# Kernel tuning notes

Measured on AMD Instinct MI355X. Metric: run time of the kernel, lower is better.

Reference implementation:

```python
import jax, jax.numpy as jnp
import numpy as np

N = 100000      # nodes
E = 1600000     # edges (before self loops)
F_IN = 128
HID = 128
C = 32
L = 3


def setup_inputs() -> dict:
    key = jax.random.key(0)
    k = jax.random.split(key, 7)
    x = jax.random.normal(k[0], (N, F_IN), dtype=jnp.float32)
    edge_index = jax.random.randint(k[1], (2, E), 0, N)
    norm = jax.random.uniform(k[2], (E + N,), dtype=jnp.float32)  # per-edge Jaccard norm incl. self loops
    # layer weights stored as [in, out] (equivalent to nn.Linear weight transposed)
    Ws = jax.random.normal(k[3], (L, HID, HID), dtype=jnp.float32) * (1.0 / np.sqrt(HID))
    bs = jnp.zeros((L, HID), dtype=jnp.float32)
    Wc = jax.random.normal(k[4], (HID, C), dtype=jnp.float32) * (1.0 / np.sqrt(HID))
    bc = jnp.zeros((C,), dtype=jnp.float32)
    return {"x": x, "edge_index": edge_index, "norm": norm,
            "Ws": Ws, "bs": bs, "Wc": Wc, "bc": bc}


def reference(x, edge_index, norm, Ws, bs, Wc, bc):
    n = x.shape[0]
    loops = jnp.arange(n, dtype=edge_index.dtype)
    src = jnp.concatenate([edge_index[0], loops])  # [E+N]
    dst = jnp.concatenate([edge_index[1], loops])  # [E+N]
    for i in range(L):
        h = x @ Ws[i]                               # [N, HID] linear (no bias)
        msg = norm[:, None] * h[src]                # edge-wise gather + scale
        agg = jax.ops.segment_max(msg, dst, num_segments=n)  # scatter-max
        agg = jnp.where(jnp.isneginf(agg), 0.0, agg)          # empty segments -> 0
        x = jax.nn.relu(agg + bs[i])
    logits = x @ Wc + bc
    return jax.nn.log_softmax(logits, axis=-1)
```

## Files before the change

kernel.cpp:

```cpp
#include <hip/hip_runtime.h>
#include <hip/hip_fp16.h>
#include <math.h>

#define HID 128
#define NCLS 32
#define BCAP 12288
#define SCAP 9728
#define SLCSH 14

typedef _Float16 half8 __attribute__((ext_vector_type(8)));
typedef _Float16 h2 __attribute__((ext_vector_type(2)));
typedef float f32x4 __attribute__((ext_vector_type(4)));

union hbits_u { unsigned short u; _Float16 f; };

__device__ __forceinline__ void gload_lds16(const void* g, void* l) {
  __builtin_amdgcn_global_load_lds(
      (const __attribute__((address_space(1))) void*)g,
      (__attribute__((address_space(3))) void*)l, 16, 0, 0);
}

__device__ __forceinline__ h2 pk_max(h2 a, h2 b) {
  return __builtin_elementwise_max(a, b);
}

__device__ __forceinline__ _Float16 dec_w(unsigned e) {
  hbits_u u; u.u = (unsigned short)((e >> 16) & 0xFFFEu);
  return u.f;
}

__global__ void k_prep_w(const float* __restrict__ Ws, __half* __restrict__ Wt,
                         int total) {
  int i = blockIdx.x * blockDim.x + threadIdx.x;
  if (i >= total) return;
  int l = i >> 14, r = i & 16383;
  int nn = r >> 7, k = r & 127;
  Wt[i] = __float2half_rn(Ws[(l << 14) + k * HID + nn]);
}

__global__ __launch_bounds__(1024) void k_bin(const int* __restrict__ ei,
                                              const float* __restrict__ norm,
                                              int* __restrict__ bucket_cur,
                                              int2* __restrict__ bins,
                                              int E, int T) {
  __shared__ int bcnt[256];
  __shared__ int bbase[256];
  int tid = threadIdx.x;
  if (tid < 256) bcnt[tid] = 0;
  __syncthreads();
  int base = blockIdx.x * 8192;
  int2 ent[8];
  int bk[8];
  #pragma unroll
  for (int i = 0; i < 8; ++i) {
    int e = base + (i << 10) + tid;
    bk[i] = -1;
    if (e < T) {
      int src, dst;
      if (e < E) { src = ei[e]; dst = ei[E + e]; } else { src = dst = e - E; }
      bk[i] = dst >> 9;
      ent[i] = make_int2(src | ((dst & 511) << 17), __float_as_int(norm[e]));
      atomicAdd(&bcnt[bk[i]], 1);
    }
  }
  __syncthreads();
  if (tid < 256) {
    int c = bcnt[tid];
    bbase[tid] = c ? atomicAdd(&bucket_cur[tid], c) : 0;
    bcnt[tid] = 0;
  }
  __syncthreads();
  #pragma unroll
  for (int i = 0; i < 8; ++i) {
    if (bk[i] >= 0) {
      int pos = bbase[bk[i]] + atomicAdd(&bcnt[bk[i]], 1);
      bins[(size_t)bk[i] * BCAP + pos] = ent[i];
    }
  }
}

__global__ __launch_bounds__(256) void k_bscan(const int* __restrict__ bucket_cur,
                                               int* __restrict__ bucket_off, int nb) {
  __shared__ int a[256];
  int tid = threadIdx.x;
  int orig = (tid < nb) ? bucket_cur[tid] : 0;
  a[tid] = orig;
  __syncthreads();
  for (int d = 1; d < 256; d <<= 1) {
    int t = (tid >= d) ? a[tid - d] : 0;
    __syncthreads();
    a[tid] += t;
    __syncthreads();
  }
  if (tid < nb) bucket_off[tid] = a[tid] - orig;
  if (tid == nb - 1) bucket_off[nb] = a[tid];
}

__global__ __launch_bounds__(1024) void k_sortbucket(
    const int2* __restrict__ bins, const int* __restrict__ bucket_off,
    unsigned* __restrict__ csr4, int* __restrict__ row_off, int n, int nb) {
  __shared__ unsigned sorted[SCAP];
  __shared__ int cnt_[4096];
  __shared__ int wsum[16];
  int b = blockIdx.x, tid = threadIdx.x;
  int goff = bucket_off[b];
  int cnt = bucket_off[b + 1] - goff;
  if (cnt > SCAP) cnt = SCAP;
  const int2* src = bins + (size_t)b * BCAP;
  int2 myent[10];
  int mykey[10];
  #pragma unroll
  for (int i = 0; i < 10; ++i) {
    int j = tid + (i << 10);
    if (j < cnt) {
      myent[i] = src[j];
      int s = myent[i].x & 0x1FFFF;
      int dl = ((unsigned)myent[i].x) >> 17;
      mykey[i] = (dl << 3) | (s >> SLCSH);
    }
  }
  #pragma unroll
  for (int i = 0; i < 4; ++i) cnt_[tid + (i << 10)] = 0;
  __syncthreads();
  #pragma unroll
  for (int i = 0; i < 10; ++i) {
    int j = tid + (i << 10);
    if (j < cnt) atomicAdd(&cnt_[mykey[i]], 1);
  }
  __syncthreads();
  int base = tid << 2;
  int l0 = cnt_[base], l1 = cnt_[base + 1], l2 = cnt_[base + 2], l3 = cnt_[base + 3];
  int s0 = l0 + l1 + l2 + l3;
  int lane = tid & 63, wid = tid >> 6;
  int incl = s0;
  #pragma unroll
  for (int d = 1; d < 64; d <<= 1) {
    int t = __shfl_up(incl, d, 64);
    if (lane >= d) incl += t;
  }
  if (lane == 63) wsum[wid] = incl;
  __syncthreads();
  if (wid == 0 && lane < 16) {
    int wv = wsum[lane];
    int winc = wv;
    #pragma unroll
    for (int d = 1; d < 16; d <<= 1) {
      int t = __shfl_up(winc, d, 16);
      if (lane >= d) winc += t;
    }
    wsum[lane] = winc - wv;
  }
  __syncthreads();
  int excl = incl - s0 + wsum[wid];
  cnt_[base]     = excl;
  cnt_[base + 1] = excl + l0;
  cnt_[base + 2] = excl + l0 + l1;
  cnt_[base + 3] = excl + l0 + l1 + l2;
  __syncthreads();
  int node = (b << 9) + tid;
  if (tid < 512 && node < n) row_off[node] = goff + cnt_[tid << 3];
  if (b == nb - 1 && tid == 0) row_off[n] = bucket_off[nb];
  __syncthreads();
  #pragma unroll
  for (int i = 0; i < 10; ++i) {
    int j = tid + (i << 10);
    if (j < cnt) {
      int pos = atomicAdd(&cnt_[mykey[i]], 1);
      if (pos < SCAP) {
        __half h = __float2half_rn(__int_as_float(myent[i].y));
        unsigned short hb = *(unsigned short*)&h;
        sorted[pos] = (unsigned)(myent[i].x & 0x1FFFF) | ((unsigned)(hb >> 1) << 17);
      }
    }
  }
  __syncthreads();
  for (int j = tid; j < cnt; j += 1024) csr4[goff + j] = sorted[j];
}

__global__ __launch_bounds__(256) void k_gemm_mfma(const __half* __restrict__ X,
                                                   const __half* __restrict__ Wl,
                                                   __half* __restrict__ H, int n) {
  __shared__ char lds[49152];
  char* ldsW = lds;
  char* ldsX = lds + 32768;
  int tid = threadIdx.x, lane = tid & 63, w = tid >> 6;
  int row0 = blockIdx.x * 64;
  int rows = n - row0; if (rows > 64) rows = 64;
  int vbytes = rows << 8;

  #pragma unroll
  for (int it = 0; it < 8; ++it) {
    int d = (w << 13) + (it << 10) + (lane << 4);
    int src = d ^ (((d >> 8) & 7) << 4);
    gload_lds16((const char*)Wl + src, ldsW + (w << 13) + (it << 10));
  }
  #pragma unroll
  for (int it = 0; it < 4; ++it) {
    int d = (w << 12) + (it << 10) + (lane << 4);
    if (d < vbytes) {
      int src = d ^ (((d >> 8) & 7) << 4);
      gload_lds16((const char*)X + ((size_t)row0 << 8) + src,
                  ldsX + (w << 12) + (it << 10));
    }
  }
  __syncthreads();

  int l15 = lane & 15, lhi = lane >> 4;
  half8 a[4];
  #pragma unroll
  for (int s = 0; s < 4; ++s) {
    int m = (w << 4) + l15;
    int d = (m << 8) + (s << 6) + (lhi << 4);
    a[s] = *(const half8*)(ldsX + (d ^ ((m & 7) << 4)));
  }
  __syncthreads();
  f32x4 acc[8] = {};
  #pragma unroll
  for (int s = 0; s < 4; ++s) {
    #pragma unroll
    for (int t = 0; t < 8; ++t) {
      int nn = (t << 4) + l15;
      int d = (nn << 8) + (s << 6) + (lhi << 4);
      half8 b = *(const half8*)(ldsW + (d ^ ((nn & 7) << 4)));
      acc[t] = __builtin_amdgcn_mfma_f32_16x16x32_f16(a[s], b, acc[t], 0, 0, 0);
    }
  }
  #pragma unroll
  for (int t = 0; t < 8; ++t) {
    #pragma unroll
    for (int r = 0; r < 4; ++r) {
      int row = (w << 4) + (lhi << 2) + r;
      int byt = (row << 8) + (t << 5) + (l15 << 1);
      *(__half*)(ldsX + (byt ^ ((row & 7) << 4))) = __float2half_rn(acc[t][r]);
    }
  }
  __syncthreads();
  #pragma unroll
  for (int it = 0; it < 4; ++it) {
    int g = ((it << 8) + tid) << 4;
    if (g < vbytes) {
      uint4 v = *(const uint4*)(ldsX + (g ^ (((g >> 8) & 7) << 4)));
      *(uint4*)((char*)H + ((size_t)row0 << 8) + g) = v;
    }
  }
}

__global__ __launch_bounds__(256) void k_gemm_mfma_f32(const float* __restrict__ X,
                                                       const __half* __restrict__ Wl,
                                                       __half* __restrict__ H, int n) {
  __shared__ char lds[65536];
  char* ldsW = lds;
  char* ldsX = lds + 32768;
  int tid = threadIdx.x, lane = tid & 63, w = tid >> 6;
  int row0 = blockIdx.x * 64;
  int rows = n - row0; if (rows > 64) rows = 64;
  int vbytes32 = rows << 9;
  int vbytes = rows << 8;

  #pragma unroll
  for (int it = 0; it < 8; ++it) {
    int d = (w << 13) + (it << 10) + (lane << 4);
    int src = d ^ (((d >> 8) & 7) << 4);
    gload_lds16((const char*)Wl + src, ldsW + (w << 13) + (it << 10));
  }
  #pragma unroll
  for (int it = 0; it < 8; ++it) {
    int d = (w << 13) + (it << 10) + (lane << 4);
    if (d < vbytes32) {
      int src = d ^ (((d >> 9) & 7) << 4);
      gload_lds16((const char*)X + ((size_t)row0 << 9) + src,
                  ldsX + (w << 13) + (it << 10));
    }
  }
  __syncthreads();

  int l15 = lane & 15, lhi = lane >> 4;
  half8 a[4];
  #pragma unroll
  for (int s = 0; s < 4; ++s) {
    int m = (w << 4) + l15;
    int d0 = (m << 9) + (s << 7) + (lhi << 5);
    int x0 = d0 ^ (((d0 >> 9) & 7) << 4);
    int d1 = d0 + 16;
    int x1 = d1 ^ (((d1 >> 9) & 7) << 4);
    float4 lo = *(const float4*)(ldsX + x0);
    float4 hi = *(const float4*)(ldsX + x1);
    half8 af;
    af[0] = (_Float16)lo.x; af[1] = (_Float16)lo.y;
    af[2] = (_Float16)lo.z; af[3] = (_Float16)lo.w;
    af[4] = (_Float16)hi.x; af[5] = (_Float16)hi.y;
    af[6] = (_Float16)hi.z; af[7] = (_Float16)hi.w;
    a[s] = af;
  }
  __syncthreads();
  f32x4 acc[8] = {};
  #pragma unroll
  for (int s = 0; s < 4; ++s) {
    #pragma unroll
    for (int t = 0; t < 8; ++t) {
      int nn = (t << 4) + l15;
      int d = (nn << 8) + (s << 6) + (lhi << 4);
      half8 b = *(const half8*)(ldsW + (d ^ ((nn & 7) << 4)));
      acc[t] = __builtin_amdgcn_mfma_f32_16x16x32_f16(a[s], b, acc[t], 0, 0, 0);
    }
  }
  #pragma unroll
  for (int t = 0; t < 8; ++t) {
    #pragma unroll
    for (int r = 0; r < 4; ++r) {
      int row = (w << 4) + (lhi << 2) + r;
      int byt = (row << 8) + (t << 5) + (l15 << 1);
      *(__half*)(ldsX + (byt ^ ((row & 7) << 4))) = __float2half_rn(acc[t][r]);
    }
  }
  __syncthreads();
  #pragma unroll
  for (int it = 0; it < 4; ++it) {
    int g = ((it << 8) + tid) << 4;
    if (g < vbytes) {
      uint4 v = *(const uint4*)(ldsX + (g ^ (((g >> 8) & 7) << 4)));
      *(uint4*)((char*)H + ((size_t)row0 << 8) + g) = v;
    }
  }
}

__global__ __launch_bounds__(256) void k_aggregate(
    const __half* __restrict__ H, const int* __restrict__ row_off,
    const unsigned* __restrict__ csr4, const float* __restrict__ bias,
    __half* __restrict__ Xout, int n) {
  int node = (int)((blockIdx.x * blockDim.x + threadIdx.x) >> 6);
  if (node >= n) return;
  int lane = threadIdx.x & 63;
  int q = lane >> 4, l4 = lane & 15;
  int beg = row_off[node], end = row_off[node + 1];
  const char* Hb = (const char*)H + (l4 << 4);
  const unsigned NEG = 0xFC00FC00u;
  h2 m0 = *(const h2*)&NEG, m1 = m0, m2 = m0, m3 = m0;
  int j = beg + q;
  for (; j + 12 < end; j += 16) {
    unsigned e0 = csr4[j], e1 = csr4[j + 4], e2 = csr4[j + 8], e3 = csr4[j + 12];
    _Float16 w0 = dec_w(e0), w1 = dec_w(e1), w2 = dec_w(e2), w3 = dec_w(e3);
    uint4 r0 = *(const uint4*)(Hb + ((size_t)(e0 & 0x1FFFF) << 8));
    uint4 r1 = *(const uint4*)(Hb + ((size_t)(e1 & 0x1FFFF) << 8));
    uint4 r2 = *(const uint4*)(Hb + ((size_t)(e2 & 0x1FFFF) << 8));
    uint4 r3 = *(const uint4*)(Hb + ((size_t)(e3 & 0x1FFFF) << 8));
    m0 = pk_max(m0, *(h2*)&r0.x * w0);
    m1 = pk_max(m1, *(h2*)&r0.y * w0);
    m2 = pk_max(m2, *(h2*)&r0.z * w0);
    m3 = pk_max(m3, *(h2*)&r0.w * w0);
    m0 = pk_max(m0, *(h2*)&r1.x * w1);
    m1 = pk_max(m1, *(h2*)&r1.y * w1);
    m2 = pk_max(m2, *(h2*)&r1.z * w1);
    m3 = pk_max(m3, *(h2*)&r1.w * w1);
    m0 = pk_max(m0, *(h2*)&r2.x * w2);
    m1 = pk_max(m1, *(h2*)&r2.y * w2);
    m2 = pk_max(m2, *(h2*)&r2.z * w2);
    m3 = pk_max(m3, *(h2*)&r2.w * w2);
    m0 = pk_max(m0, *(h2*)&r3.x * w3);
    m1 = pk_max(m1, *(h2*)&r3.y * w3);
    m2 = pk_max(m2, *(h2*)&r3.z * w3);
    m3 = pk_max(m3, *(h2*)&r3.w * w3);
  }
  for (; j < end; j += 4) {
    unsigned e0 = csr4[j];
    _Float16 w0 = dec_w(e0);
    uint4 r0 = *(const uint4*)(Hb + ((size_t)(e0 & 0x1FFFF) << 8));
    m0 = pk_max(m0, *(h2*)&r0.x * w0);
    m1 = pk_max(m1, *(h2*)&r0.y * w0);
    m2 = pk_max(m2, *(h2*)&r0.z * w0);
    m3 = pk_max(m3, *(h2*)&r0.w * w0);
  }
  #pragma unroll
  for (int d = 16; d <= 32; d <<= 1) {
    unsigned u0 = __shfl_xor(*(unsigned*)&m0, d, 64);
    unsigned u1 = __shfl_xor(*(unsigned*)&m1, d, 64);
    unsigned u2 = __shfl_xor(*(unsigned*)&m2, d, 64);
    unsigned u3 = __shfl_xor(*(unsigned*)&m3, d, 64);
    m0 = pk_max(m0, *(h2*)&u0);
    m1 = pk_max(m1, *(h2*)&u1);
    m2 = pk_max(m2, *(h2*)&u2);
    m3 = pk_max(m3, *(h2*)&u3);
  }
  if (q == 0) {
    float f0x = (float)m0.x, f0y = (float)m0.y;
    float f1x = (float)m1.x, f1y = (float)m1.y;
    float f2x = (float)m2.x, f2y = (float)m2.y;
    float f3x = (float)m3.x, f3y = (float)m3.y;
    if (end == beg) {
      f0x=f0y=f1x=f1y=f2x=f2y=f3x=f3y = 0.f;
    }
    float4 b0 = ((const float4*)bias)[l4 << 1];
    float4 b1 = ((const float4*)bias)[(l4 << 1) + 1];
    __half2 o0 = __floats2half2_rn(fmaxf(f0x + b0.x, 0.f), fmaxf(f0y + b0.y, 0.f));
    __half2 o1 = __floats2half2_rn(fmaxf(f1x + b0.z, 0.f), fmaxf(f1y + b0.w, 0.f));
    __half2 o2 = __floats2half2_rn(fmaxf(f2x + b1.x, 0.f), fmaxf(f2y + b1.y, 0.f));
    __half2 o3 = __floats2half2_rn(fmaxf(f3x + b1.z, 0.f), fmaxf(f3y + b1.w, 0.f));
    uint4 ov = make_uint4(*(unsigned*)&o0, *(unsigned*)&o1,
                          *(unsigned*)&o2, *(unsigned*)&o3);
    *(uint4*)((char*)Xout + ((size_t)node << 8) + (l4 << 4)) = ov;
  }
}

__global__ __launch_bounds__(256) void k_classifier(
    const __half* __restrict__ X, const float* __restrict__ Wc,
    const float* __restrict__ bc, float* __restrict__ out, int n) {
  __shared__ float sW[HID * NCLS];
  __shared__ float sx[8][HID];
  int tid = threadIdx.x;
  #pragma unroll
  for (int i = 0; i < 4; ++i)
    ((float4*)sW)[tid + 256 * i] = ((const float4*)Wc)[tid + 256 * i];
  int node0 = blockIdx.x * 8;
  {
    int r = tid >> 5, c = (tid & 31) << 2;
    if (node0 + r < n) {
      __half2 p0 = *(const __half2*)&X[(size_t)(node0 + r) * HID + c];
      __half2 p1 = *(const __half2*)&X[(size_t)(node0 + r) * HID + c + 2];
      float2 f0 = __half22float2(p0), f1 = __half22float2(p1);
      sx[r][c] = f0.x; sx[r][c + 1] = f0.y; sx[r][c + 2] = f1.x; sx[r][c + 3] = f1.y;
    }
  }
  __syncthreads();
  int g = tid >> 5, c = tid & 31;
  int node = node0 + g;
  if (node >= n) return;
  float acc = bc[c];
  #pragma unroll 8
  for (int k = 0; k < HID; ++k)
    acc = fmaf(sx[g][k], sW[k * NCLS + c], acc);
  float m = acc;
  #pragma unroll
  for (int off = 16; off; off >>= 1) m = fmaxf(m, __shfl_xor(m, off, 32));
  float e = expf(acc - m);
  float s = e;
  #pragma unroll
  for (int off = 16; off; off >>= 1) s += __shfl_xor(s, off, 32);
  out[(size_t)node * NCLS + c] = acc - m - logf(s);
}

extern "C" void kernel_launch(void* const* d_in, const int* in_sizes, int n_in,
                              void* d_out, int out_size, void* d_ws, size_t ws_size,
                              hipStream_t stream) {
  const float* x    = (const float*)d_in[0];
  const int*   ei   = (const int*)d_in[1];
  const float* norm = (const float*)d_in[2];
  const float* Ws   = (const float*)d_in[3];
  const float* bs   = (const float*)d_in[4];
  const float* Wc   = (const float*)d_in[5];
  const float* bc   = (const float*)d_in[6];
  float* out = (float*)d_out;

  const int N = in_sizes[0] / HID;
  const int E = in_sizes[1] / 2;
  const int L = in_sizes[3] / (HID * HID);
  const int T = E + N;
  const int NB = (N + 511) >> 9;

  char* p = (char*)d_ws;
  auto alloc = [&](size_t bytes) {
    char* r = p; p += (bytes + 255) & ~(size_t)255; return r;
  };
  __half*   xb0        = (__half*)alloc((size_t)N * HID * 2);
  __half*   xb1        = (__half*)alloc((size_t)N * HID * 2);
  __half*   hbuf       = (__half*)alloc((size_t)N * HID * 2);
  __half*   Wt         = (__half*)alloc((size_t)L * HID * HID * 2);
  int*      row_off    = (int*)alloc(((size_t)N + 1) * 4);
  int*      bucket_cur = (int*)alloc(256 * 4);
  int*      bucket_off = (int*)alloc(257 * 4);
  int2*     bins       = (int2*)alloc((size_t)NB * BCAP * 8);
  unsigned* csr4       = (unsigned*)alloc((size_t)T * 4);
  (void)ws_size; (void)n_in; (void)out_size;

  hipMemsetAsync(bucket_cur, 0, 256 * 4, stream);
  k_prep_w<<<(L * HID * HID + 255) / 256, 256, 0, stream>>>(Ws, Wt, L * HID * HID);
  k_bin<<<(T + 8191) / 8192, 1024, 0, stream>>>(ei, norm, bucket_cur, bins, E, T);
  k_bscan<<<1, 256, 0, stream>>>(bucket_cur, bucket_off, NB);
  k_sortbucket<<<NB, 1024, 0, stream>>>(bins, bucket_off, csr4, row_off, N, NB);

  const int GB = (N + 63) / 64;
  k_gemm_mfma_f32<<<GB, 256, 0, stream>>>(x, Wt, hbuf, N);
  k_aggregate<<<(N + 3) / 4, 256, 0, stream>>>(
      hbuf, row_off, csr4, bs, xb0, N);
  k_gemm_mfma<<<GB, 256, 0, stream>>>(xb0, Wt + (size_t)HID * HID, hbuf, N);
  k_aggregate<<<(N + 3) / 4, 256, 0, stream>>>(
      hbuf, row_off, csr4, bs + HID, xb1, N);
  k_gemm_mfma<<<GB, 256, 0, stream>>>(xb1, Wt + (size_t)2 * HID * HID, hbuf, N);
  k_aggregate<<<(N + 3) / 4, 256, 0, stream>>>(
      hbuf, row_off, csr4, bs + 2 * HID, xb0, N);
  k_classifier<<<(N + 7) / 8, 256, 0, stream>>>(xb0, Wc, bc, out, N);
}
```

Measured before the change: 313.6 us.

## Fuse classifier into last aggregation, fold bucket scan into sort, drop source sub-sort

Merges the final aggregation with the classifier and log-softmax, so each node's 128-wide feature stays in registers and the last hidden activation buffer is never written or re-read. The separate single-block bucket scan kernel is removed: every sort block now computes the prefix over the bucket counts itself. The within-bucket sort key no longer sub-sorts each destination's edges by source slice, which makes sorting cheaper but may reduce gather locality in the aggregation. The classifier weights are pre-transposed in the weight-prep kernel so the fused kernel can do the projection with per-lane partial dot products and cross-lane shuffle reductions.

```diff
diff --git a/kernel.cpp b/kernel.cpp
--- a/kernel.cpp
+++ b/kernel.cpp
@@ -6,7 +6,6 @@
 #define NCLS 32
 #define BCAP 12288
 #define SCAP 9728
-#define SLCSH 14
 
 typedef _Float16 half8 __attribute__((ext_vector_type(8)));
 typedef _Float16 h2 __attribute__((ext_vector_type(2)));
@@ -29,13 +28,19 @@
   return u.f;
 }
 
-__global__ void k_prep_w(const float* __restrict__ Ws, __half* __restrict__ Wt,
-                         int total) {
+__global__ void k_prep_w(const float* __restrict__ Ws, const float* __restrict__ Wc,
+                         __half* __restrict__ Wt, float* __restrict__ Wct,
+                         int totalW, int totalC) {
   int i = blockIdx.x * blockDim.x + threadIdx.x;
-  if (i >= total) return;
-  int l = i >> 14, r = i & 16383;
-  int nn = r >> 7, k = r & 127;
-  Wt[i] = __float2half_rn(Ws[(l << 14) + k * HID + nn]);
+  if (i < totalW) {
+    int l = i >> 14, r = i & 16383;
+    int nn = r >> 7, k = r & 127;
+    Wt[i] = __float2half_rn(Ws[(l << 14) + k * HID + nn]);
+  } else if (i < totalW + totalC) {
+    int j = i - totalW;
+    int c = j >> 7, ch = j & 127;
+    Wct[j] = Wc[ch * NCLS + c];
+  }
 }
 
 __global__ __launch_bounds__(1024) void k_bin(const int* __restrict__ ei,
@@ -79,97 +84,74 @@
   }
 }
 
-__global__ __launch_bounds__(256) void k_bscan(const int* __restrict__ bucket_cur,
-                                               int* __restrict__ bucket_off, int nb) {
-  __shared__ int a[256];
-  int tid = threadIdx.x;
-  int orig = (tid < nb) ? bucket_cur[tid] : 0;
-  a[tid] = orig;
+__global__ __launch_bounds__(1024) void k_sortbucket(
+    const int2* __restrict__ bins, const int* __restrict__ bucket_cur,
+    unsigned* __restrict__ csr4, int* __restrict__ row_off,
+    int n, int nb, int T) {
+  __shared__ unsigned sorted[SCAP];
+  __shared__ int scnt[512];
+  __shared__ int wsum[8];
+  __shared__ int bscan[256];
+  int b = blockIdx.x, tid = threadIdx.x;
+  if (tid < 256) bscan[tid] = (tid < nb) ? bucket_cur[tid] : 0;
   __syncthreads();
   for (int d = 1; d < 256; d <<= 1) {
-    int t = (tid >= d) ? a[tid - d] : 0;
+    int t = (tid < 256 && tid >= d) ? bscan[tid - d] : 0;
     __syncthreads();
-    a[tid] += t;
+    if (tid < 256) bscan[tid] += t;
     __syncthreads();
   }
-  if (tid < nb) bucket_off[tid] = a[tid] - orig;
-  if (tid == nb - 1) bucket_off[nb] = a[tid];
-}
-
-__global__ __launch_bounds__(1024) void k_sortbucket(
-    const int2* __restrict__ bins, const int* __restrict__ bucket_off,
-    unsigned* __restrict__ csr4, int* __restrict__ row_off, int n, int nb) {
-  __shared__ unsigned sorted[SCAP];
-  __shared__ int cnt_[4096];
-  __shared__ int wsum[16];
-  int b = blockIdx.x, tid = threadIdx.x;
-  int goff = bucket_off[b];
-  int cnt = bucket_off[b + 1] - goff;
-  if (cnt > SCAP) cnt = SCAP;
+  int cntb = bucket_cur[b];
+  int goff = bscan[b] - cntb;
+  int cnt = cntb > SCAP ? SCAP : cntb;
   const int2* src = bins + (size_t)b * BCAP;
   int2 myent[10];
-  int mykey[10];
+  #pragma unroll
+  for (int i = 0; i < 10; ++i) {
+    int j = tid + (i << 10);
+    if (j < cnt) myent[i] = src[j];
+  }
+  if (tid < 512) scnt[tid] = 0;
+  __syncthreads();
+  #pragma unroll
+  for (int i = 0; i < 10; ++i) {
+    int j = tid + (i << 10);
+    if (j < cnt) atomicAdd(&scnt[((unsigned)myent[i].x) >> 17], 1);
+  }
+  __syncthreads();
+  int lane = tid & 63, wid = tid >> 6;
+  int v = (tid < 512) ? scnt[tid] : 0;
+  int incl = v;
+  #pragma unroll
+  for (int d = 1; d < 64; d <<= 1) {
+    int t = __shfl_up(incl, d, 64);
+    if (lane >= d) incl += t;
+  }
+  if (tid < 512 && lane == 63) wsum[wid] = incl;
+  __syncthreads();
+  if (tid == 0) {
+    int s = 0;
+    #pragma unroll
+    for (int i = 0; i < 8; ++i) { int t = wsum[i]; wsum[i] = s; s += t; }
+  }
+  __syncthreads();
+  int excl = incl - v + ((tid < 512) ? wsum[wid] : 0);
+  int node = (b << 9) + tid;
+  if (tid < 512 && node < n) row_off[node] = goff + excl;
+  if (b == nb - 1 && tid == 0) row_off[n] = T;
+  __syncthreads();
+  if (tid < 512) scnt[tid] = excl;
+  __syncthreads();
   #pragma unroll
   for (int i = 0; i < 10; ++i) {
     int j = tid + (i << 10);
     if (j < cnt) {
-      myent[i] = src[j];
-      int s = myent[i].x & 0x1FFFF;
-      int dl = ((unsigned)myent[i].x) >> 17;
-      mykey[i] = (dl << 3) | (s >> SLCSH);
-    }
-  }
-  #pragma unroll
-  for (int i = 0; i < 4; ++i) cnt_[tid + (i << 10)] = 0;
-  __syncthreads();
-  #pragma unroll
-  for (int i = 0; i < 10; ++i) {
-    int j = tid + (i << 10);
-    if (j < cnt) atomicAdd(&cnt_[mykey[i]], 1);
-  }
-  __syncthreads();
-  int base = tid << 2;
-  int l0 = cnt_[base], l1 = cnt_[base + 1], l2 = cnt_[base + 2], l3 = cnt_[base + 3];
-  int s0 = l0 + l1 + l2 + l3;
-  int lane = tid & 63, wid = tid >> 6;
-  int incl = s0;
-  #pragma unroll
-  for (int d = 1; d < 64; d <<= 1) {
-    int t = __shfl_up(incl, d, 64);
-    if (lane >= d) incl += t;
-  }
-  if (lane == 63) wsum[wid] = incl;
-  __syncthreads();
-  if (wid == 0 && lane < 16) {
-    int wv = wsum[lane];
-    int winc = wv;
-    #pragma unroll
-    for (int d = 1; d < 16; d <<= 1) {
-      int t = __shfl_up(winc, d, 16);
-      if (lane >= d) winc += t;
-    }
-    wsum[lane] = winc - wv;
-  }
-  __syncthreads();
-  int excl = incl - s0 + wsum[wid];
-  cnt_[base]     = excl;
-  cnt_[base + 1] = excl + l0;
-  cnt_[base + 2] = excl + l0 + l1;
-  cnt_[base + 3] = excl + l0 + l1 + l2;
-  __syncthreads();
-  int node = (b << 9) + tid;
-  if (tid < 512 && node < n) row_off[node] = goff + cnt_[tid << 3];
-  if (b == nb - 1 && tid == 0) row_off[n] = bucket_off[nb];
-  __syncthreads();
-  #pragma unroll
-  for (int i = 0; i < 10; ++i) {
-    int j = tid + (i << 10);
-    if (j < cnt) {
-      int pos = atomicAdd(&cnt_[mykey[i]], 1);
+      int2 e = myent[i];
+      int pos = atomicAdd(&scnt[((unsigned)e.x) >> 17], 1);
       if (pos < SCAP) {
-        __half h = __float2half_rn(__int_as_float(myent[i].y));
+        __half h = __float2half_rn(__int_as_float(e.y));
         unsigned short hb = *(unsigned short*)&h;
-        sorted[pos] = (unsigned)(myent[i].x & 0x1FFFF) | ((unsigned)(hb >> 1) << 17);
+        sorted[pos] = (unsigned)(e.x & 0x1FFFF) | ((unsigned)(hb >> 1) << 17);
       }
     }
   }
@@ -324,71 +306,72 @@
   }
 }
 
+#define AGG_GATHER                                                             \
+  int lane = threadIdx.x & 63;                                                 \
+  int q = lane >> 4, l4 = lane & 15;                                           \
+  int beg = row_off[node], end = row_off[node + 1];                            \
+  const char* Hb = (const char*)H + (l4 << 4);                                 \
+  const unsigned NEG = 0xFC00FC00u;                                            \
+  h2 m0 = *(const h2*)&NEG, m1 = m0, m2 = m0, m3 = m0;                         \
+  int j = beg + q;                                                             \
+  for (; j + 12 < end; j += 16) {                                              \
+    unsigned e0 = csr4[j], e1 = csr4[j + 4], e2 = csr4[j + 8], e3 = csr4[j + 12]; \
+    _Float16 w0 = dec_w(e0), w1 = dec_w(e1), w2 = dec_w(e2), w3 = dec_w(e3);   \
+    uint4 r0 = *(const uint4*)(Hb + ((size_t)(e0 & 0x1FFFF) << 8));            \
+    uint4 r1 = *(const uint4*)(Hb + ((size_t)(e1 & 0x1FFFF) << 8));            \
+    uint4 r2 = *(const uint4*)(Hb + ((size_t)(e2 & 0x1FFFF) << 8));            \
+    uint4 r3 = *(const uint4*)(Hb + ((size_t)(e3 & 0x1FFFF) << 8));            \
+    m0 = pk_max(m0, *(h2*)&r0.x * w0);                                         \
+    m1 = pk_max(m1, *(h2*)&r0.y * w0);                                         \
+    m2 = pk_max(m2, *(h2*)&r0.z * w0);                                         \
+    m3 = pk_max(m3, *(h2*)&r0.w * w0);                                         \
+    m0 = pk_max(m0, *(h2*)&r1.x * w1);                                         \
+    m1 = pk_max(m1, *(h2*)&r1.y * w1);                                         \
+    m2 = pk_max(m2, *(h2*)&r1.z * w1);                                         \
+    m3 = pk_max(m3, *(h2*)&r1.w * w1);                                         \
+    m0 = pk_max(m0, *(h2*)&r2.x * w2);                                         \
+    m1 = pk_max(m1, *(h2*)&r2.y * w2);                                         \
+    m2 = pk_max(m2, *(h2*)&r2.z * w2);                                         \
+    m3 = pk_max(m3, *(h2*)&r2.w * w2);                                         \
+    m0 = pk_max(m0, *(h2*)&r3.x * w3);                                         \
+    m1 = pk_max(m1, *(h2*)&r3.y * w3);                                         \
+    m2 = pk_max(m2, *(h2*)&r3.z * w3);                                         \
+    m3 = pk_max(m3, *(h2*)&r3.w * w3);                                         \
+  }                                                                            \
+  for (; j < end; j += 4) {                                                    \
+    unsigned e0 = csr4[j];                                                     \
+    _Float16 w0 = dec_w(e0);                                                   \
+    uint4 r0 = *(const uint4*)(Hb + ((size_t)(e0 & 0x1FFFF) << 8));            \
+    m0 = pk_max(m0, *(h2*)&r0.x * w0);                                         \
+    m1 = pk_max(m1, *(h2*)&r0.y * w0);                                         \
+    m2 = pk_max(m2, *(h2*)&r0.z * w0);                                         \
+    m3 = pk_max(m3, *(h2*)&r0.w * w0);                                         \
+  }                                                                            \
+  _Pragma("unroll")                                                            \
+  for (int d = 16; d <= 32; d <<= 1) {                                         \
+    unsigned u0 = __shfl_xor(*(unsigned*)&m0, d, 64);                          \
+    unsigned u1 = __shfl_xor(*(unsigned*)&m1, d, 64);                          \
+    unsigned u2 = __shfl_xor(*(unsigned*)&m2, d, 64);                          \
+    unsigned u3 = __shfl_xor(*(unsigned*)&m3, d, 64);                          \
+    m0 = pk_max(m0, *(h2*)&u0);                                                \
+    m1 = pk_max(m1, *(h2*)&u1);                                                \
+    m2 = pk_max(m2, *(h2*)&u2);                                                \
+    m3 = pk_max(m3, *(h2*)&u3);                                                \
+  }
+
 __global__ __launch_bounds__(256) void k_aggregate(
     const __half* __restrict__ H, const int* __restrict__ row_off,
     const unsigned* __restrict__ csr4, const float* __restrict__ bias,
     __half* __restrict__ Xout, int n) {
   int node = (int)((blockIdx.x * blockDim.x + threadIdx.x) >> 6);
   if (node >= n) return;
-  int lane = threadIdx.x & 63;
-  int q = lane >> 4, l4 = lane & 15;
-  int beg = row_off[node], end = row_off[node + 1];
-  const char* Hb = (const char*)H + (l4 << 4);
-  const unsigned NEG = 0xFC00FC00u;
-  h2 m0 = *(const h2*)&NEG, m1 = m0, m2 = m0, m3 = m0;
-  int j = beg + q;
-  for (; j + 12 < end; j += 16) {
-    unsigned e0 = csr4[j], e1 = csr4[j + 4], e2 = csr4[j + 8], e3 = csr4[j + 12];
-    _Float16 w0 = dec_w(e0), w1 = dec_w(e1), w2 = dec_w(e2), w3 = dec_w(e3);
-    uint4 r0 = *(const uint4*)(Hb + ((size_t)(e0 & 0x1FFFF) << 8));
-    uint4 r1 = *(const uint4*)(Hb + ((size_t)(e1 & 0x1FFFF) << 8));
-    uint4 r2 = *(const uint4*)(Hb + ((size_t)(e2 & 0x1FFFF) << 8));
-    uint4 r3 = *(const uint4*)(Hb + ((size_t)(e3 & 0x1FFFF) << 8));
-    m0 = pk_max(m0, *(h2*)&r0.x * w0);
-    m1 = pk_max(m1, *(h2*)&r0.y * w0);
-    m2 = pk_max(m2, *(h2*)&r0.z * w0);
-    m3 = pk_max(m3, *(h2*)&r0.w * w0);
-    m0 = pk_max(m0, *(h2*)&r1.x * w1);
-    m1 = pk_max(m1, *(h2*)&r1.y * w1);
-    m2 = pk_max(m2, *(h2*)&r1.z * w1);
-    m3 = pk_max(m3, *(h2*)&r1.w * w1);
-    m0 = pk_max(m0, *(h2*)&r2.x * w2);
-    m1 = pk_max(m1, *(h2*)&r2.y * w2);
-    m2 = pk_max(m2, *(h2*)&r2.z * w2);
-    m3 = pk_max(m3, *(h2*)&r2.w * w2);
-    m0 = pk_max(m0, *(h2*)&r3.x * w3);
-    m1 = pk_max(m1, *(h2*)&r3.y * w3);
-    m2 = pk_max(m2, *(h2*)&r3.z * w3);
-    m3 = pk_max(m3, *(h2*)&r3.w * w3);
-  }
-  for (; j < end; j += 4) {
-    unsigned e0 = csr4[j];
-    _Float16 w0 = dec_w(e0);
-    uint4 r0 = *(const uint4*)(Hb + ((size_t)(e0 & 0x1FFFF) << 8));
-    m0 = pk_max(m0, *(h2*)&r0.x * w0);
-    m1 = pk_max(m1, *(h2*)&r0.y * w0);
-    m2 = pk_max(m2, *(h2*)&r0.z * w0);
-    m3 = pk_max(m3, *(h2*)&r0.w * w0);
-  }
-  #pragma unroll
-  for (int d = 16; d <= 32; d <<= 1) {
-    unsigned u0 = __shfl_xor(*(unsigned*)&m0, d, 64);
-    unsigned u1 = __shfl_xor(*(unsigned*)&m1, d, 64);
-    unsigned u2 = __shfl_xor(*(unsigned*)&m2, d, 64);
-    unsigned u3 = __shfl_xor(*(unsigned*)&m3, d, 64);
-    m0 = pk_max(m0, *(h2*)&u0);
-    m1 = pk_max(m1, *(h2*)&u1);
-    m2 = pk_max(m2, *(h2*)&u2);
-    m3 = pk_max(m3, *(h2*)&u3);
-  }
+  AGG_GATHER
   if (q == 0) {
     float f0x = (float)m0.x, f0y = (float)m0.y;
     float f1x = (float)m1.x, f1y = (float)m1.y;
     float f2x = (float)m2.x, f2y = (float)m2.y;
     float f3x = (float)m3.x, f3y = (float)m3.y;
-    if (end == beg) {
-      f0x=f0y=f1x=f1y=f2x=f2y=f3x=f3y = 0.f;
-    }
+    if (end == beg) { f0x=f0y=f1x=f1y=f2x=f2y=f3x=f3y = 0.f; }
     float4 b0 = ((const float4*)bias)[l4 << 1];
     float4 b1 = ((const float4*)bias)[(l4 << 1) + 1];
     __half2 o0 = __floats2half2_rn(fmaxf(f0x + b0.x, 0.f), fmaxf(f0y + b0.y, 0.f));
@@ -401,41 +384,63 @@
   }
 }
 
-__global__ __launch_bounds__(256) void k_classifier(
-    const __half* __restrict__ X, const float* __restrict__ Wc,
-    const float* __restrict__ bc, float* __restrict__ out, int n) {
-  __shared__ float sW[HID * NCLS];
-  __shared__ float sx[8][HID];
-  int tid = threadIdx.x;
-  #pragma unroll
-  for (int i = 0; i < 4; ++i)
-    ((float4*)sW)[tid + 256 * i] = ((const float4*)Wc)[tid + 256 * i];
-  int node0 = blockIdx.x * 8;
+__global__ __launch_bounds__(256) void k_aggregate_cls(
+    const __half* __restrict__ H, const int* __restrict__ row_off,
+    const unsigned* __restrict__ csr4, const float* __restrict__ bias,
+    const float* __restrict__ Wct, const float* __restrict__ bc,
+    float* __restrict__ out, int n) {
+  int node = (int)((blockIdx.x * blockDim.x + threadIdx.x) >> 6);
+  if (node >= n) return;
+  AGG_GATHER
+  float xv[8];
+  xv[0] = (float)m0.x; xv[1] = (float)m0.y;
+  xv[2] = (float)m1.x; xv[3] = (float)m1.y;
+  xv[4] = (float)m2.x; xv[5] = (float)m2.y;
+  xv[6] = (float)m3.x; xv[7] = (float)m3.y;
+  if (end == beg) {
+    #pragma unroll
+    for (int k = 0; k < 8; ++k) xv[k] = 0.f;
+  }
   {
-    int r = tid >> 5, c = (tid & 31) << 2;
-    if (node0 + r < n) {
-      __half2 p0 = *(const __half2*)&X[(size_t)(node0 + r) * HID + c];
-      __half2 p1 = *(const __half2*)&X[(size_t)(node0 + r) * HID + c + 2];
-      float2 f0 = __half22float2(p0), f1 = __half22float2(p1);
-      sx[r][c] = f0.x; sx[r][c + 1] = f0.y; sx[r][c + 2] = f1.x; sx[r][c + 3] = f1.y;
-    }
-  }
-  __syncthreads();
-  int g = tid >> 5, c = tid & 31;
-  int node = node0 + g;
-  if (node >= n) return;
-  float acc = bc[c];
-  #pragma unroll 8
-  for (int k = 0; k < HID; ++k)
-    acc = fmaf(sx[g][k], sW[k * NCLS + c], acc);
-  float m = acc;
-  #pragma unroll
-  for (int off = 16; off; off >>= 1) m = fmaxf(m, __shfl_xor(m, off, 32));
-  float e = expf(acc - m);
-  float s = e;
-  #pragma unroll
-  for (int off = 16; off; off >>= 1) s += __shfl_xor(s, off, 32);
-  out[(size_t)node * NCLS + c] = acc - m - logf(s);
+    float4 b0 = ((const float4*)bias)[l4 << 1];
+    float4 b1 = ((const float4*)bias)[(l4 << 1) + 1];
+    xv[0] = fmaxf(xv[0] + b0.x, 0.f); xv[1] = fmaxf(xv[1] + b0.y, 0.f);
+    xv[2] = fmaxf(xv[2] + b0.z, 0.f); xv[3] = fmaxf(xv[3] + b0.w, 0.f);
+    xv[4] = fmaxf(xv[4] + b1.x, 0.f); xv[5] = fmaxf(xv[5] + b1.y, 0.f);
+    xv[6] = fmaxf(xv[6] + b1.z, 0.f); xv[7] = fmaxf(xv[7] + b1.w, 0.f);
+  }
+  float lg[8];
+  #pragma unroll
+  for (int t = 0; t < 8; ++t) {
+    const float4* wp = (const float4*)(Wct + (((q << 3) + t) << 7) + (l4 << 3));
+    float4 wa = wp[0], wb = wp[1];
+    float s = xv[0] * wa.x + xv[1] * wa.y + xv[2] * wa.z + xv[3] * wa.w;
+    s += xv[4] * wb.x + xv[5] * wb.y + xv[6] * wb.z + xv[7] * wb.w;
+    lg[t] = s;
+  }
+  #pragma unroll
+  for (int d = 1; d <= 8; d <<= 1) {
+    #pragma unroll
+    for (int t = 0; t < 8; ++t) lg[t] += __shfl_xor(lg[t], d, 64);
+  }
+  #pragma unroll
+  for (int t = 0; t < 8; ++t) lg[t] += bc[(q << 3) + t];
+  float mx = lg[0];
+  #pragma unroll
+  for (int t = 1; t < 8; ++t) mx = fmaxf(mx, lg[t]);
+  mx = fmaxf(mx, __shfl_xor(mx, 16, 64));
+  mx = fmaxf(mx, __shfl_xor(mx, 32, 64));
+  float se = 0.f;
+  #pragma unroll
+  for (int t = 0; t < 8; ++t) se += expf(lg[t] - mx);
+  se += __shfl_xor(se, 16, 64);
+  se += __shfl_xor(se, 32, 64);
+  float ls = logf(se) + mx;
+  if (l4 == 0) {
+    float* dst = out + (size_t)node * NCLS + (q << 3);
+    *(float4*)dst = make_float4(lg[0] - ls, lg[1] - ls, lg[2] - ls, lg[3] - ls);
+    *(float4*)(dst + 4) = make_float4(lg[4] - ls, lg[5] - ls, lg[6] - ls, lg[7] - ls);
+  }
 }
 
 extern "C" void kernel_launch(void* const* d_in, const int* in_sizes, int n_in,
@@ -464,28 +469,27 @@
   __half*   xb1        = (__half*)alloc((size_t)N * HID * 2);
   __half*   hbuf       = (__half*)alloc((size_t)N * HID * 2);
   __half*   Wt         = (__half*)alloc((size_t)L * HID * HID * 2);
+  float*    Wct        = (float*)alloc((size_t)HID * NCLS * 4);
   int*      row_off    = (int*)alloc(((size_t)N + 1) * 4);
   int*      bucket_cur = (int*)alloc(256 * 4);
-  int*      bucket_off = (int*)alloc(257 * 4);
   int2*     bins       = (int2*)alloc((size_t)NB * BCAP * 8);
   unsigned* csr4       = (unsigned*)alloc((size_t)T * 4);
   (void)ws_size; (void)n_in; (void)out_size;
 
+  const int totalW = L * HID * HID;
+  const int totalC = HID * NCLS;
   hipMemsetAsync(bucket_cur, 0, 256 * 4, stream);
-  k_prep_w<<<(L * HID * HID + 255) / 256, 256, 0, stream>>>(Ws, Wt, L * HID * HID);
+  k_prep_w<<<(totalW + totalC + 255) / 256, 256, 0, stream>>>(
+      Ws, Wc, Wt, Wct, totalW, totalC);
   k_bin<<<(T + 8191) / 8192, 1024, 0, stream>>>(ei, norm, bucket_cur, bins, E, T);
-  k_bscan<<<1, 256, 0, stream>>>(bucket_cur, bucket_off, NB);
-  k_sortbucket<<<NB, 1024, 0, stream>>>(bins, bucket_off, csr4, row_off, N, NB);
+  k_sortbucket<<<NB, 1024, 0, stream>>>(bins, bucket_cur, csr4, row_off, N, NB, T);
 
   const int GB = (N + 63) / 64;
   k_gemm_mfma_f32<<<GB, 256, 0, stream>>>(x, Wt, hbuf, N);
-  k_aggregate<<<(N + 3) / 4, 256, 0, stream>>>(
-      hbuf, row_off, csr4, bs, xb0, N);
+  k_aggregate<<<(N + 3) / 4, 256, 0, stream>>>(hbuf, row_off, csr4, bs, xb0, N);
   k_gemm_mfma<<<GB, 256, 0, stream>>>(xb0, Wt + (size_t)HID * HID, hbuf, N);
-  k_aggregate<<<(N + 3) / 4, 256, 0, stream>>>(
-      hbuf, row_off, csr4, bs + HID, xb1, N);
+  k_aggregate<<<(N + 3) / 4, 256, 0, stream>>>(hbuf, row_off, csr4, bs + HID, xb1, N);
   k_gemm_mfma<<<GB, 256, 0, stream>>>(xb1, Wt + (size_t)2 * HID * HID, hbuf, N);
-  k_aggregate<<<(N + 3) / 4, 256, 0, stream>>>(
-      hbuf, row_off, csr4, bs + 2 * HID, xb0, N);
-  k_classifier<<<(N + 7) / 8, 256, 0, stream>>>(xb0, Wc, bc, out, N);
-}
+  k_aggregate_cls<<<(N + 3) / 4, 256, 0, stream>>>(
+      hbuf, row_off, csr4, bs + 2 * HID, Wct, bc, out, N);
+}
```

Result: no change. 313.3 us (-0.1%).

## Use MFMA classifier, fold bucket scan into sort, drop source-slice sort key

Applied to the files above, without the earlier changes.

Replaces the scalar FP32 classifier with an MFMA f16 kernel over 64-row tiles, loading swizzled X and a transposed half-precision Wc into LDS, with the log-softmax done in registers. The separate bucket-scan launch is removed and each sort block redoes the 256-entry prefix scan itself. Edges within a bucket are now sorted only by destination, no longer also by source slice, which shrinks the counting histogram but gives up source-locality ordering within each row for the aggregate gathers. Casting Wc to half adds a small precision change.

```diff
diff --git a/kernel.cpp b/kernel.cpp
--- a/kernel.cpp
+++ b/kernel.cpp
@@ -6,7 +6,6 @@
 #define NCLS 32
 #define BCAP 12288
 #define SCAP 9728
-#define SLCSH 14
 
 typedef _Float16 half8 __attribute__((ext_vector_type(8)));
 typedef _Float16 h2 __attribute__((ext_vector_type(2)));
@@ -29,13 +28,19 @@
   return u.f;
 }
 
-__global__ void k_prep_w(const float* __restrict__ Ws, __half* __restrict__ Wt,
-                         int total) {
+__global__ void k_prep_w(const float* __restrict__ Ws, const float* __restrict__ Wc,
+                         __half* __restrict__ Wt, __half* __restrict__ Wch,
+                         int totalW, int totalC) {
   int i = blockIdx.x * blockDim.x + threadIdx.x;
-  if (i >= total) return;
-  int l = i >> 14, r = i & 16383;
-  int nn = r >> 7, k = r & 127;
-  Wt[i] = __float2half_rn(Ws[(l << 14) + k * HID + nn]);
+  if (i < totalW) {
+    int l = i >> 14, r = i & 16383;
+    int nn = r >> 7, k = r & 127;
+    Wt[i] = __float2half_rn(Ws[(l << 14) + k * HID + nn]);
+  } else if (i < totalW + totalC) {
+    int j = i - totalW;
+    int c = j >> 7, k = j & 127;
+    Wch[j] = __float2half_rn(Wc[k * NCLS + c]);
+  }
 }
 
 __global__ __launch_bounds__(1024) void k_bin(const int* __restrict__ ei,
@@ -79,97 +84,74 @@
   }
 }
 
-__global__ __launch_bounds__(256) void k_bscan(const int* __restrict__ bucket_cur,
-                                               int* __restrict__ bucket_off, int nb) {
-  __shared__ int a[256];
-  int tid = threadIdx.x;
-  int orig = (tid < nb) ? bucket_cur[tid] : 0;
-  a[tid] = orig;
+__global__ __launch_bounds__(1024) void k_sortbucket(
+    const int2* __restrict__ bins, const int* __restrict__ bucket_cur,
+    unsigned* __restrict__ csr4, int* __restrict__ row_off,
+    int n, int nb, int T) {
+  __shared__ unsigned sorted[SCAP];
+  __shared__ int scnt[512];
+  __shared__ int wsum[8];
+  __shared__ int bscan[256];
+  int b = blockIdx.x, tid = threadIdx.x;
+  if (tid < 256) bscan[tid] = (tid < nb) ? bucket_cur[tid] : 0;
   __syncthreads();
   for (int d = 1; d < 256; d <<= 1) {
-    int t = (tid >= d) ? a[tid - d] : 0;
+    int t = (tid < 256 && tid >= d) ? bscan[tid - d] : 0;
     __syncthreads();
-    a[tid] += t;
+    if (tid < 256) bscan[tid] += t;
     __syncthreads();
   }
-  if (tid < nb) bucket_off[tid] = a[tid] - orig;
-  if (tid == nb - 1) bucket_off[nb] = a[tid];
-}
-
-__global__ __launch_bounds__(1024) void k_sortbucket(
-    const int2* __restrict__ bins, const int* __restrict__ bucket_off,
-    unsigned* __restrict__ csr4, int* __restrict__ row_off, int n, int nb) {
-  __shared__ unsigned sorted[SCAP];
-  __shared__ int cnt_[4096];
-  __shared__ int wsum[16];
-  int b = blockIdx.x, tid = threadIdx.x;
-  int goff = bucket_off[b];
-  int cnt = bucket_off[b + 1] - goff;
-  if (cnt > SCAP) cnt = SCAP;
+  int cntb = bucket_cur[b];
+  int goff = bscan[b] - cntb;
+  int cnt = cntb > SCAP ? SCAP : cntb;
   const int2* src = bins + (size_t)b * BCAP;
   int2 myent[10];
-  int mykey[10];
+  #pragma unroll
+  for (int i = 0; i < 10; ++i) {
+    int j = tid + (i << 10);
+    if (j < cnt) myent[i] = src[j];
+  }
+  if (tid < 512) scnt[tid] = 0;
+  __syncthreads();
+  #pragma unroll
+  for (int i = 0; i < 10; ++i) {
+    int j = tid + (i << 10);
+    if (j < cnt) atomicAdd(&scnt[((unsigned)myent[i].x) >> 17], 1);
+  }
+  __syncthreads();
+  int lane = tid & 63, wid = tid >> 6;
+  int v = (tid < 512) ? scnt[tid] : 0;
+  int incl = v;
+  #pragma unroll
+  for (int d = 1; d < 64; d <<= 1) {
+    int t = __shfl_up(incl, d, 64);
+    if (lane >= d) incl += t;
+  }
+  if (tid < 512 && lane == 63) wsum[wid] = incl;
+  __syncthreads();
+  if (tid == 0) {
+    int s = 0;
+    #pragma unroll
+    for (int i = 0; i < 8; ++i) { int t = wsum[i]; wsum[i] = s; s += t; }
+  }
+  __syncthreads();
+  int excl = incl - v + ((tid < 512) ? wsum[wid] : 0);
+  int node = (b << 9) + tid;
+  if (tid < 512 && node < n) row_off[node] = goff + excl;
+  if (b == nb - 1 && tid == 0) row_off[n] = T;
+  __syncthreads();
+  if (tid < 512) scnt[tid] = excl;
+  __syncthreads();
   #pragma unroll
   for (int i = 0; i < 10; ++i) {
     int j = tid + (i << 10);
     if (j < cnt) {
-      myent[i] = src[j];
-      int s = myent[i].x & 0x1FFFF;
-      int dl = ((unsigned)myent[i].x) >> 17;
-      mykey[i] = (dl << 3) | (s >> SLCSH);
-    }
-  }
-  #pragma unroll
-  for (int i = 0; i < 4; ++i) cnt_[tid + (i << 10)] = 0;
-  __syncthreads();
-  #pragma unroll
-  for (int i = 0; i < 10; ++i) {
-    int j = tid + (i << 10);
-    if (j < cnt) atomicAdd(&cnt_[mykey[i]], 1);
-  }
-  __syncthreads();
-  int base = tid << 2;
-  int l0 = cnt_[base], l1 = cnt_[base + 1], l2 = cnt_[base + 2], l3 = cnt_[base + 3];
-  int s0 = l0 + l1 + l2 + l3;
-  int lane = tid & 63, wid = tid >> 6;
-  int incl = s0;
-  #pragma unroll
-  for (int d = 1; d < 64; d <<= 1) {
-    int t = __shfl_up(incl, d, 64);
-    if (lane >= d) incl += t;
-  }
-  if (lane == 63) wsum[wid] = incl;
-  __syncthreads();
-  if (wid == 0 && lane < 16) {
-    int wv = wsum[lane];
-    int winc = wv;
-    #pragma unroll
-    for (int d = 1; d < 16; d <<= 1) {
-      int t = __shfl_up(winc, d, 16);
-      if (lane >= d) winc += t;
-    }
-    wsum[lane] = winc - wv;
-  }
-  __syncthreads();
-  int excl = incl - s0 + wsum[wid];
-  cnt_[base]     = excl;
-  cnt_[base + 1] = excl + l0;
-  cnt_[base + 2] = excl + l0 + l1;
-  cnt_[base + 3] = excl + l0 + l1 + l2;
-  __syncthreads();
-  int node = (b << 9) + tid;
-  if (tid < 512 && node < n) row_off[node] = goff + cnt_[tid << 3];
-  if (b == nb - 1 && tid == 0) row_off[n] = bucket_off[nb];
-  __syncthreads();
-  #pragma unroll
-  for (int i = 0; i < 10; ++i) {
-    int j = tid + (i << 10);
-    if (j < cnt) {
-      int pos = atomicAdd(&cnt_[mykey[i]], 1);
+      int2 e = myent[i];
+      int pos = atomicAdd(&scnt[((unsigned)e.x) >> 17], 1);
       if (pos < SCAP) {
-        __half h = __float2half_rn(__int_as_float(myent[i].y));
+        __half h = __float2half_rn(__int_as_float(e.y));
         unsigned short hb = *(unsigned short*)&h;
-        sorted[pos] = (unsigned)(myent[i].x & 0x1FFFF) | ((unsigned)(hb >> 1) << 17);
+        sorted[pos] = (unsigned)(e.x & 0x1FFFF) | ((unsigned)(hb >> 1) << 17);
       }
     }
   }
@@ -386,9 +368,7 @@
     float f1x = (float)m1.x, f1y = (float)m1.y;
     float f2x = (float)m2.x, f2y = (float)m2.y;
     float f3x = (float)m3.x, f3y = (float)m3.y;
-    if (end == beg) {
-      f0x=f0y=f1x=f1y=f2x=f2y=f3x=f3y = 0.f;
-    }
+    if (end == beg) { f0x=f0y=f1x=f1y=f2x=f2y=f3x=f3y = 0.f; }
     float4 b0 = ((const float4*)bias)[l4 << 1];
     float4 b1 = ((const float4*)bias)[(l4 << 1) + 1];
     __half2 o0 = __floats2half2_rn(fmaxf(f0x + b0.x, 0.f), fmaxf(f0y + b0.y, 0.f));
@@ -401,41 +381,66 @@
   }
 }
 
-__global__ __launch_bounds__(256) void k_classifier(
-    const __half* __restrict__ X, const float* __restrict__ Wc,
+__global__ __launch_bounds__(256) void k_classifier_mfma(
+    const __half* __restrict__ X, const __half* __restrict__ Wch,
     const float* __restrict__ bc, float* __restrict__ out, int n) {
-  __shared__ float sW[HID * NCLS];
-  __shared__ float sx[8][HID];
-  int tid = threadIdx.x;
-  #pragma unroll
-  for (int i = 0; i < 4; ++i)
-    ((float4*)sW)[tid + 256 * i] = ((const float4*)Wc)[tid + 256 * i];
-  int node0 = blockIdx.x * 8;
-  {
-    int r = tid >> 5, c = (tid & 31) << 2;
-    if (node0 + r < n) {
-      __half2 p0 = *(const __half2*)&X[(size_t)(node0 + r) * HID + c];
-      __half2 p1 = *(const __half2*)&X[(size_t)(node0 + r) * HID + c + 2];
-      float2 f0 = __half22float2(p0), f1 = __half22float2(p1);
-      sx[r][c] = f0.x; sx[r][c + 1] = f0.y; sx[r][c + 2] = f1.x; sx[r][c + 3] = f1.y;
-    }
-  }
-  __syncthreads();
-  int g = tid >> 5, c = tid & 31;
-  int node = node0 + g;
-  if (node >= n) return;
-  float acc = bc[c];
-  #pragma unroll 8
-  for (int k = 0; k < HID; ++k)
-    acc = fmaf(sx[g][k], sW[k * NCLS + c], acc);
-  float m = acc;
-  #pragma unroll
-  for (int off = 16; off; off >>= 1) m = fmaxf(m, __shfl_xor(m, off, 32));
-  float e = expf(acc - m);
-  float s = e;
-  #pragma unroll
-  for (int off = 16; off; off >>= 1) s += __shfl_xor(s, off, 32);
-  out[(size_t)node * NCLS + c] = acc - m - logf(s);
+  __shared__ char lds[24576];
+  char* ldsW = lds;
+  char* ldsX = lds + 8192;
+  int tid = threadIdx.x, lane = tid & 63, w = tid >> 6;
+  int row0 = blockIdx.x * 64;
+  int rows = n - row0; if (rows > 64) rows = 64;
+  int vbytes = rows << 8;
+  #pragma unroll
+  for (int it = 0; it < 2; ++it) {
+    int d = (it << 12) + (w << 10) + (lane << 4);
+    int src = d ^ (((d >> 8) & 7) << 4);
+    gload_lds16((const char*)Wch + src, ldsW + (it << 12) + (w << 10));
+  }
+  #pragma unroll
+  for (int it = 0; it < 4; ++it) {
+    int d = (w << 12) + (it << 10) + (lane << 4);
+    if (d < vbytes) {
+      int src = d ^ (((d >> 8) & 7) << 4);
+      gload_lds16((const char*)X + ((size_t)row0 << 8) + src,
+                  ldsX + (w << 12) + (it << 10));
+    }
+  }
+  __syncthreads();
+  int l15 = lane & 15, lhi = lane >> 4;
+  f32x4 acc[2] = {};
+  #pragma unroll
+  for (int s = 0; s < 4; ++s) {
+    int m = (w << 4) + l15;
+    int d = (m << 8) + (s << 6) + (lhi << 4);
+    half8 a = *(const half8*)(ldsX + (d ^ ((m & 7) << 4)));
+    #pragma unroll
+    for (int t = 0; t < 2; ++t) {
+      int nn = (t << 4) + l15;
+      int dw = (nn << 8) + (s << 6) + (lhi << 4);
+      half8 b = *(const half8*)(ldsW + (dw ^ ((nn & 7) << 4)));
+      acc[t] = __builtin_amdgcn_mfma_f32_16x16x32_f16(a, b, acc[t], 0, 0, 0);
+    }
+  }
+  float bc0 = bc[l15], bc1 = bc[l15 + 16];
+  #pragma unroll
+  for (int r = 0; r < 4; ++r) {
+    int row = (w << 4) + (lhi << 2) + r;
+    float lg0 = acc[0][r] + bc0;
+    float lg1 = acc[1][r] + bc1;
+    float mx = fmaxf(lg0, lg1);
+    #pragma unroll
+    for (int d = 1; d <= 8; d <<= 1) mx = fmaxf(mx, __shfl_xor(mx, d, 64));
+    float se = expf(lg0 - mx) + expf(lg1 - mx);
+    #pragma unroll
+    for (int d = 1; d <= 8; d <<= 1) se += __shfl_xor(se, d, 64);
+    float ls = logf(se) + mx;
+    int gnode = row0 + row;
+    if (gnode < n) {
+      out[(size_t)gnode * NCLS + l15] = lg0 - ls;
+      out[(size_t)gnode * NCLS + l15 + 16] = lg1 - ls;
+    }
+  }
 }
 
 extern "C" void kernel_launch(void* const* d_in, const int* in_sizes, int n_in,
@@ -464,28 +469,27 @@
   __half*   xb1        = (__half*)alloc((size_t)N * HID * 2);
   __half*   hbuf       = (__half*)alloc((size_t)N * HID * 2);
   __half*   Wt         = (__half*)alloc((size_t)L * HID * HID * 2);
+  __half*   Wch        = (__half*)alloc((size_t)HID * NCLS * 2);
   int*      row_off    = (int*)alloc(((size_t)N + 1) * 4);
   int*      bucket_cur = (int*)alloc(256 * 4);
-  int*      bucket_off = (int*)alloc(257 * 4);
   int2*     bins       = (int2*)alloc((size_t)NB * BCAP * 8);
   unsigned* csr4       = (unsigned*)alloc((size_t)T * 4);
   (void)ws_size; (void)n_in; (void)out_size;
 
+  const int totalW = L * HID * HID;
+  const int totalC = HID * NCLS;
   hipMemsetAsync(bucket_cur, 0, 256 * 4, stream);
-  k_prep_w<<<(L * HID * HID + 255) / 256, 256, 0, stream>>>(Ws, Wt, L * HID * HID);
+  k_prep_w<<<(totalW + totalC + 255) / 256, 256, 0, stream>>>(
+      Ws, Wc, Wt, Wch, totalW, totalC);
   k_bin<<<(T + 8191) / 8192, 1024, 0, stream>>>(ei, norm, bucket_cur, bins, E, T);
-  k_bscan<<<1, 256, 0, stream>>>(bucket_cur, bucket_off, NB);
-  k_sortbucket<<<NB, 1024, 0, stream>>>(bins, bucket_off, csr4, row_off, N, NB);
+  k_sortbucket<<<NB, 1024, 0, stream>>>(bins, bucket_cur, csr4, row_off, N, NB, T);
 
   const int GB = (N + 63) / 64;
   k_gemm_mfma_f32<<<GB, 256, 0, stream>>>(x, Wt, hbuf, N);
-  k_aggregate<<<(N + 3) / 4, 256, 0, stream>>>(
-      hbuf, row_off, csr4, bs, xb0, N);
+  k_aggregate<<<(N + 3) / 4, 256, 0, stream>>>(hbuf, row_off, csr4, bs, xb0, N);
   k_gemm_mfma<<<GB, 256, 0, stream>>>(xb0, Wt + (size_t)HID * HID, hbuf, N);
-  k_aggregate<<<(N + 3) / 4, 256, 0, stream>>>(
-      hbuf, row_off, csr4, bs + HID, xb1, N);
+  k_aggregate<<<(N + 3) / 4, 256, 0, stream>>>(hbuf, row_off, csr4, bs + HID, xb1, N);
   k_gemm_mfma<<<GB, 256, 0, stream>>>(xb1, Wt + (size_t)2 * HID * HID, hbuf, N);
-  k_aggregate<<<(N + 3) / 4, 256, 0, stream>>>(
-      hbuf, row_off, csr4, bs + 2 * HID, xb0, N);
-  k_classifier<<<(N + 7) / 8, 256, 0, stream>>>(xb0, Wc, bc, out, N);
-}
+  k_aggregate<<<(N + 3) / 4, 256, 0, stream>>>(hbuf, row_off, csr4, bs + 2 * HID, xb0, N);
+  k_classifier_mfma<<<GB, 256, 0, stream>>>(xb0, Wch, bc, out, N);
+}
```

Result: faster. 276.2 us (-11.9%).
